# Kernel tuning notes

Measured on AMD Instinct MI355X. Metric: run time of the kernel, lower is better.

Reference implementation:

```python
import jax, jax.numpy as jnp
import numpy as np


def setup_inputs() -> dict:
    key = jax.random.key(0)
    k_u, k_ev, k_lam = jax.random.split(key, 3)
    B, K, L = 64, 32, 8192
    u = jax.random.normal(k_u, (B, L), dtype=jnp.float32)
    # synthetic stand-in for load_or_compute_eigen_data
    eigenvectors = jax.random.normal(k_ev, (K, L), dtype=jnp.float32)
    # module stores eigenvalues ** 0.25
    eigenvalues = jax.random.uniform(k_lam, (K,), dtype=jnp.float32) ** 0.25
    return {"u": u, "eigenvectors": eigenvectors, "eigenvalues": eigenvalues}


def reference(u, eigenvectors, eigenvalues):
    L = u.shape[-1]
    u_fft = jnp.fft.rfft(u)                    # (B, L//2+1) complex
    ev_fft = jnp.fft.rfft(eigenvectors)        # (K, L//2+1) complex (precomputed param in torch)
    # NOTE: faithful to torch einsum 'bi,kj->bkj' which SUMS over i
    p_fft = jnp.einsum('bi,kj->bkj', u_fft, ev_fft)   # (B, K, L//2+1)
    convolutions = jnp.fft.irfft(p_fft, n=L)           # (B, K, L)
    result = jnp.einsum('bkl,k->bl', convolutions, eigenvalues)  # (B, L)
    return result
```

## Files before the change

kernel.cpp:

```cpp
#include <hip/hip_runtime.h>
#include <math.h>

constexpr int Lc = 8192;
constexpr int Kc = 32;
constexpr int Bc = 64;
constexpr int NSLICE = 32;
constexpr int NCHUNK = 8;

__device__ inline float cot_pi_frac_f(int d) {
    int dd = d; float s = 1.0f;
    if (dd > Lc / 2) { dd = Lc - dd; s = -1.0f; }
    float ang = (float)(M_PI * (double)dd / (double)Lc);
    return s * __fdividef(__cosf(ang), __sinf(ang));
}


__global__ __launch_bounds__(256) void k_w(
    const float* __restrict__ ev, const float* __restrict__ lam,
    float* __restrict__ wbuf)
{
    const int n = blockIdx.x * 256 + threadIdx.x;
    float wv = 0.f;
#pragma unroll
    for (int k = 0; k < Kc; ++k)
        wv = fmaf(lam[k], ev[(size_t)k * Lc + n], wv);
    wbuf[n] = wv;
}

__global__ __launch_bounds__(256) void k_main(
    const float* __restrict__ u, const float* __restrict__ wbuf,
    float* __restrict__ sr, float* __restrict__ si2, float* __restrict__ Bp)
{
    const int t = threadIdx.x;

    if (blockIdx.x < 64) {
        int b = blockIdx.x;
        const float4* u4 = (const float4*)(u + (size_t)b * Lc);
        float ar0 = 0.f, ar1 = 0.f, ai0 = 0.f, ai1 = 0.f;
#pragma unroll
        for (int i = 0; i < 8; ++i) {
            int j = t + 256 * i;
            float4 v = u4[j];
            ar0 += v.x; ar1 += v.z;
            ai0 = fmaf(v.y, cot_pi_frac_f(4 * j + 1), ai0);
            ai1 = fmaf(v.w, cot_pi_frac_f(4 * j + 3), ai1);
        }
        if (t == 0) ar0 += 4096.0f * u[(size_t)b * Lc];
        float ar = ar0 + ar1, ai = ai0 + ai1;
        for (int off = 32; off > 0; off >>= 1) {
            ar += __shfl_down(ar, off);
            ai += __shfl_down(ai, off);
        }
        __shared__ float red[8];
        int wave = t >> 6, lane = t & 63;
        if (lane == 0) { red[wave] = ar; red[4 + wave] = ai; }
        __syncthreads();
        if (t == 0) {
            sr[b]  = red[0] + red[1] + red[2] + red[3];
            si2[b] = (2.0f / (float)Lc) * (red[4] + red[5] + red[6] + red[7]);
        }
        return;
    }

    __shared__ float s_we[643];
    __shared__ float s_wo[643];
    __shared__ __align__(16) float s_c[128];

    const int blk = blockIdx.x - 64;
    const int cn = blk & (NCHUNK - 1);
    const int sl = blk >> 3;
    const int n0 = cn * 1024;
    const int dbase = sl * 256;
    const int A = n0 - dbase - 256;

#pragma unroll
    for (int it = 0; it < 2; ++it) {
        int gq = t + 256 * it;
        if (gq < 320) {
            int pos = (A + 4 * gq + 2 * Lc) & (Lc - 1);
            float4 v = *(const float4*)(wbuf + pos);
            s_we[2 * gq]     = v.x; s_wo[2 * gq]     = v.y;
            s_we[2 * gq + 1] = v.z; s_wo[2 * gq + 1] = v.w;
        }
    }
    if (t < 128) s_c[t] = cot_pi_frac_f(dbase + 255 - 2 * t);
    __syncthreads();

    const int g = t >> 1, p = t & 1;
    const float* s_wp = p ? (s_we + 1) : s_wo;
    const int jb = 4 * g;

    float W0 = s_wp[jb],     W1 = s_wp[jb + 1], W2 = s_wp[jb + 2], W3 = s_wp[jb + 3];
    float W4 = s_wp[jb + 4], W5 = s_wp[jb + 5], W6 = s_wp[jb + 6];
    float a0 = 0.f, a1 = 0.f, a2 = 0.f, a3 = 0.f;

    const float4* s_c4 = (const float4*)s_c;
#pragma unroll
    for (int G = 0; G < 32; ++G) {
        const int mm0 = 4 * G;
        float4 cv = s_c4[G];
        a0 = fmaf(cv.x, W0, a0); a1 = fmaf(cv.x, W1, a1); a2 = fmaf(cv.x, W2, a2); a3 = fmaf(cv.x, W3, a3);
        a0 = fmaf(cv.y, W1, a0); a1 = fmaf(cv.y, W2, a1); a2 = fmaf(cv.y, W3, a2); a3 = fmaf(cv.y, W4, a3);
        a0 = fmaf(cv.z, W2, a0); a1 = fmaf(cv.z, W3, a1); a2 = fmaf(cv.z, W4, a2); a3 = fmaf(cv.z, W5, a3);
        a0 = fmaf(cv.w, W3, a0); a1 = fmaf(cv.w, W4, a1); a2 = fmaf(cv.w, W5, a2); a3 = fmaf(cv.w, W6, a3);
        if (G < 31) {
            W0 = W4; W1 = W5; W2 = W6;
            W3 = s_wp[jb + mm0 + 7];  W4 = s_wp[jb + mm0 + 8];
            W5 = s_wp[jb + mm0 + 9];  W6 = s_wp[jb + mm0 + 10];
        }
    }
    float* dst = Bp + (size_t)sl * Lc + n0 + 8 * g + p;
    dst[0] = a0; dst[2] = a1; dst[4] = a2; dst[6] = a3;
}

__global__ __launch_bounds__(256) void k_out(
    const float* __restrict__ wbuf,
    const float* __restrict__ sr, const float* __restrict__ si2,
    const float* __restrict__ Bp, float* __restrict__ out)
{
    __shared__ float s_sv[128];
    const int t = threadIdx.x;
    if (t < 128) s_sv[t] = (t < 64) ? sr[t] : si2[t - 64];
    const int cn = blockIdx.x & 31, bg = blockIdx.x >> 5;
    const int n = cn * 256 + t;
    float wv = wbuf[n];
    float bsum = 0.f;
#pragma unroll
    for (int s = 0; s < NSLICE; ++s) bsum += Bp[(size_t)s * Lc + n];
    __syncthreads();
#pragma unroll
    for (int j = 0; j < 8; ++j) {
        int b = bg * 8 + j;
        out[(size_t)b * Lc + n] = fmaf(s_sv[b], wv, s_sv[64 + b] * bsum);
    }
}

extern "C" void kernel_launch(void* const* d_in, const int* in_sizes, int n_in,
                              void* d_out, int out_size, void* d_ws, size_t ws_size,
                              hipStream_t stream) {
    const float* u   = (const float*)d_in[0];
    const float* ev  = (const float*)d_in[1];
    const float* lam = (const float*)d_in[2];
    float* out = (float*)d_out;

    float* ws   = (float*)d_ws;
    float* sr   = ws;
    float* si2  = ws + 64;
    float* wbuf = ws + 128;
    float* Bp   = ws + 128 + Lc;

    hipLaunchKernelGGL(k_w,    dim3(Lc / 256), dim3(256), 0, stream, ev, lam, wbuf);
    hipLaunchKernelGGL(k_main, dim3(64 + NCHUNK * NSLICE), dim3(256), 0, stream,
                       u, wbuf, sr, si2, Bp);
    hipLaunchKernelGGL(k_out,  dim3(256), dim3(256), 0, stream,
                       wbuf, sr, si2, Bp, out);
}
```

Before: 64.46 us.

## Fuse three kernels into one cooperative kernel with grid-wide syncs

Merges the weight-reduction, main correlation and output kernels into a single cooperative launch of 256 blocks, separated by two grid.sync barriers. The u-reduction blocks and the wbuf blocks now run concurrently in phase one. This removes two kernel launch boundaries and their drain/fill gaps. In exchange it adds grid-barrier cost, and the cooperative launch path can carry extra overhead.

```diff
diff --git a/kernel.cpp b/kernel.cpp
--- a/kernel.cpp
+++ b/kernel.cpp
@@ -1,5 +1,8 @@
 #include <hip/hip_runtime.h>
+#include <hip/hip_cooperative_groups.h>
 #include <math.h>
+
+namespace cg = cooperative_groups;
 
 constexpr int Lc = 8192;
 constexpr int Kc = 32;
@@ -15,26 +18,24 @@
 }
 
 
-__global__ __launch_bounds__(256) void k_w(
-    const float* __restrict__ ev, const float* __restrict__ lam,
-    float* __restrict__ wbuf)
+__global__ __launch_bounds__(256) void k_fused(
+    const float* __restrict__ u, const float* __restrict__ ev,
+    const float* __restrict__ lam, float* __restrict__ out,
+    float* __restrict__ sr, float* __restrict__ si2,
+    float* __restrict__ wbuf, float* __restrict__ Bp)
 {
-    const int n = blockIdx.x * 256 + threadIdx.x;
-    float wv = 0.f;
-#pragma unroll
-    for (int k = 0; k < Kc; ++k)
-        wv = fmaf(lam[k], ev[(size_t)k * Lc + n], wv);
-    wbuf[n] = wv;
-}
+    cg::grid_group grid = cg::this_grid();
+    const int t = threadIdx.x;
+    const int blk = blockIdx.x;
 
-__global__ __launch_bounds__(256) void k_main(
-    const float* __restrict__ u, const float* __restrict__ wbuf,
-    float* __restrict__ sr, float* __restrict__ si2, float* __restrict__ Bp)
-{
-    const int t = threadIdx.x;
+    __shared__ float s_we[643];
+    __shared__ float s_wo[643];
+    __shared__ __align__(16) float s_c[128];
+    __shared__ float red[8];
+    __shared__ float s_sv[128];
 
-    if (blockIdx.x < 64) {
-        int b = blockIdx.x;
+    if (blk < 64) {
+        const int b = blk;
         const float4* u4 = (const float4*)(u + (size_t)b * Lc);
         float ar0 = 0.f, ar1 = 0.f, ai0 = 0.f, ai1 = 0.f;
 #pragma unroll
@@ -51,7 +52,6 @@
             ar += __shfl_down(ar, off);
             ai += __shfl_down(ai, off);
         }
-        __shared__ float red[8];
         int wave = t >> 6, lane = t & 63;
         if (lane == 0) { red[wave] = ar; red[4 + wave] = ai; }
         __syncthreads();
@@ -59,79 +59,80 @@
             sr[b]  = red[0] + red[1] + red[2] + red[3];
             si2[b] = (2.0f / (float)Lc) * (red[4] + red[5] + red[6] + red[7]);
         }
-        return;
+    } else if (blk < 96) {
+        const int n = (blk - 64) * 256 + t;
+        float wv = 0.f;
+#pragma unroll
+        for (int k = 0; k < Kc; ++k)
+            wv = fmaf(lam[k], ev[(size_t)k * Lc + n], wv);
+        wbuf[n] = wv;
     }
 
-    __shared__ float s_we[643];
-    __shared__ float s_wo[643];
-    __shared__ __align__(16) float s_c[128];
+    grid.sync();
 
-    const int blk = blockIdx.x - 64;
-    const int cn = blk & (NCHUNK - 1);
-    const int sl = blk >> 3;
-    const int n0 = cn * 1024;
-    const int dbase = sl * 256;
-    const int A = n0 - dbase - 256;
+    {
+        const int cn = blk & (NCHUNK - 1);
+        const int sl = blk >> 3;
+        const int n0 = cn * 1024;
+        const int dbase = sl * 256;
+        const int A = n0 - dbase - 256;
 
 #pragma unroll
-    for (int it = 0; it < 2; ++it) {
-        int gq = t + 256 * it;
-        if (gq < 320) {
-            int pos = (A + 4 * gq + 2 * Lc) & (Lc - 1);
-            float4 v = *(const float4*)(wbuf + pos);
-            s_we[2 * gq]     = v.x; s_wo[2 * gq]     = v.y;
-            s_we[2 * gq + 1] = v.z; s_wo[2 * gq + 1] = v.w;
+        for (int it = 0; it < 2; ++it) {
+            int gq = t + 256 * it;
+            if (gq < 320) {
+                int pos = (A + 4 * gq + 2 * Lc) & (Lc - 1);
+                float4 v = *(const float4*)(wbuf + pos);
+                s_we[2 * gq]     = v.x; s_wo[2 * gq]     = v.y;
+                s_we[2 * gq + 1] = v.z; s_wo[2 * gq + 1] = v.w;
+            }
         }
+        if (t < 128) s_c[t] = cot_pi_frac_f(dbase + 255 - 2 * t);
+        __syncthreads();
+
+        const int g = t >> 1, p = t & 1;
+        const float* s_wp = p ? (s_we + 1) : s_wo;
+        const int jb = 4 * g;
+
+        float W0 = s_wp[jb],     W1 = s_wp[jb + 1], W2 = s_wp[jb + 2], W3 = s_wp[jb + 3];
+        float W4 = s_wp[jb + 4], W5 = s_wp[jb + 5], W6 = s_wp[jb + 6];
+        float a0 = 0.f, a1 = 0.f, a2 = 0.f, a3 = 0.f;
+
+        const float4* s_c4 = (const float4*)s_c;
+#pragma unroll
+        for (int G = 0; G < 32; ++G) {
+            const int mm0 = 4 * G;
+            float4 cv = s_c4[G];
+            a0 = fmaf(cv.x, W0, a0); a1 = fmaf(cv.x, W1, a1); a2 = fmaf(cv.x, W2, a2); a3 = fmaf(cv.x, W3, a3);
+            a0 = fmaf(cv.y, W1, a0); a1 = fmaf(cv.y, W2, a1); a2 = fmaf(cv.y, W3, a2); a3 = fmaf(cv.y, W4, a3);
+            a0 = fmaf(cv.z, W2, a0); a1 = fmaf(cv.z, W3, a1); a2 = fmaf(cv.z, W4, a2); a3 = fmaf(cv.z, W5, a3);
+            a0 = fmaf(cv.w, W3, a0); a1 = fmaf(cv.w, W4, a1); a2 = fmaf(cv.w, W5, a2); a3 = fmaf(cv.w, W6, a3);
+            if (G < 31) {
+                W0 = W4; W1 = W5; W2 = W6;
+                W3 = s_wp[jb + mm0 + 7];  W4 = s_wp[jb + mm0 + 8];
+                W5 = s_wp[jb + mm0 + 9];  W6 = s_wp[jb + mm0 + 10];
+            }
+        }
+        float* dst = Bp + (size_t)sl * Lc + n0 + 8 * g + p;
+        dst[0] = a0; dst[2] = a1; dst[4] = a2; dst[6] = a3;
     }
-    if (t < 128) s_c[t] = cot_pi_frac_f(dbase + 255 - 2 * t);
-    __syncthreads();
 
-    const int g = t >> 1, p = t & 1;
-    const float* s_wp = p ? (s_we + 1) : s_wo;
-    const int jb = 4 * g;
+    grid.sync();
 
-    float W0 = s_wp[jb],     W1 = s_wp[jb + 1], W2 = s_wp[jb + 2], W3 = s_wp[jb + 3];
-    float W4 = s_wp[jb + 4], W5 = s_wp[jb + 5], W6 = s_wp[jb + 6];
-    float a0 = 0.f, a1 = 0.f, a2 = 0.f, a3 = 0.f;
-
-    const float4* s_c4 = (const float4*)s_c;
+    {
+        if (t < 128) s_sv[t] = (t < 64) ? sr[t] : si2[t - 64];
+        const int cn = blk & 31, bg = blk >> 5;
+        const int n = cn * 256 + t;
+        float wv = wbuf[n];
+        float bsum = 0.f;
 #pragma unroll
-    for (int G = 0; G < 32; ++G) {
-        const int mm0 = 4 * G;
-        float4 cv = s_c4[G];
-        a0 = fmaf(cv.x, W0, a0); a1 = fmaf(cv.x, W1, a1); a2 = fmaf(cv.x, W2, a2); a3 = fmaf(cv.x, W3, a3);
-        a0 = fmaf(cv.y, W1, a0); a1 = fmaf(cv.y, W2, a1); a2 = fmaf(cv.y, W3, a2); a3 = fmaf(cv.y, W4, a3);
-        a0 = fmaf(cv.z, W2, a0); a1 = fmaf(cv.z, W3, a1); a2 = fmaf(cv.z, W4, a2); a3 = fmaf(cv.z, W5, a3);
-        a0 = fmaf(cv.w, W3, a0); a1 = fmaf(cv.w, W4, a1); a2 = fmaf(cv.w, W5, a2); a3 = fmaf(cv.w, W6, a3);
-        if (G < 31) {
-            W0 = W4; W1 = W5; W2 = W6;
-            W3 = s_wp[jb + mm0 + 7];  W4 = s_wp[jb + mm0 + 8];
-            W5 = s_wp[jb + mm0 + 9];  W6 = s_wp[jb + mm0 + 10];
+        for (int s = 0; s < NSLICE; ++s) bsum += Bp[(size_t)s * Lc + n];
+        __syncthreads();
+#pragma unroll
+        for (int j = 0; j < 8; ++j) {
+            int b = bg * 8 + j;
+            out[(size_t)b * Lc + n] = fmaf(s_sv[b], wv, s_sv[64 + b] * bsum);
         }
-    }
-    float* dst = Bp + (size_t)sl * Lc + n0 + 8 * g + p;
-    dst[0] = a0; dst[2] = a1; dst[4] = a2; dst[6] = a3;
-}
-
-__global__ __launch_bounds__(256) void k_out(
-    const float* __restrict__ wbuf,
-    const float* __restrict__ sr, const float* __restrict__ si2,
-    const float* __restrict__ Bp, float* __restrict__ out)
-{
-    __shared__ float s_sv[128];
-    const int t = threadIdx.x;
-    if (t < 128) s_sv[t] = (t < 64) ? sr[t] : si2[t - 64];
-    const int cn = blockIdx.x & 31, bg = blockIdx.x >> 5;
-    const int n = cn * 256 + t;
-    float wv = wbuf[n];
-    float bsum = 0.f;
-#pragma unroll
-    for (int s = 0; s < NSLICE; ++s) bsum += Bp[(size_t)s * Lc + n];
-    __syncthreads();
-#pragma unroll
-    for (int j = 0; j < 8; ++j) {
-        int b = bg * 8 + j;
-        out[(size_t)b * Lc + n] = fmaf(s_sv[b], wv, s_sv[64 + b] * bsum);
     }
 }
 
@@ -149,9 +150,8 @@
     float* wbuf = ws + 128;
     float* Bp   = ws + 128 + Lc;
 
-    hipLaunchKernelGGL(k_w,    dim3(Lc / 256), dim3(256), 0, stream, ev, lam, wbuf);
-    hipLaunchKernelGGL(k_main, dim3(64 + NCHUNK * NSLICE), dim3(256), 0, stream,
-                       u, wbuf, sr, si2, Bp);
-    hipLaunchKernelGGL(k_out,  dim3(256), dim3(256), 0, stream,
-                       wbuf, sr, si2, Bp, out);
+    void* args[] = { (void*)&u, (void*)&ev, (void*)&lam, (void*)&out,
+                     (void*)&sr, (void*)&si2, (void*)&wbuf, (void*)&Bp };
+    hipLaunchCooperativeKernel((void*)k_fused, dim3(256), dim3(256),
+                               args, 0, stream);
 }
```

Result: slower. 132.8 us (+106.1%).

## Regroup kernels: fuse u-reductions with w computation, vectorize conv LDS reads

Applied to the files above, without the earlier changes.

The per-batch u reductions move out of the conv kernel into a new pre-kernel that also computes the lambda-weighted eigenvector sum, so the conv kernel runs only convolution blocks. Shared-memory buffers are laid out so each thread reads its weights as aligned float4 loads from LDS instead of four scalar loads per step. The number of launches stays the same, but the reduction blocks now run alongside the w computation rather than competing with conv blocks, and the inner loop issues fewer LDS instructions.

```diff
diff --git a/kernel.cpp b/kernel.cpp
--- a/kernel.cpp
+++ b/kernel.cpp
@@ -15,24 +15,12 @@
 }
 
 
-__global__ __launch_bounds__(256) void k_w(
-    const float* __restrict__ ev, const float* __restrict__ lam,
-    float* __restrict__ wbuf)
-{
-    const int n = blockIdx.x * 256 + threadIdx.x;
-    float wv = 0.f;
-#pragma unroll
-    for (int k = 0; k < Kc; ++k)
-        wv = fmaf(lam[k], ev[(size_t)k * Lc + n], wv);
-    wbuf[n] = wv;
-}
-
-__global__ __launch_bounds__(256) void k_main(
-    const float* __restrict__ u, const float* __restrict__ wbuf,
-    float* __restrict__ sr, float* __restrict__ si2, float* __restrict__ Bp)
+__global__ __launch_bounds__(256) void k_pre(
+    const float* __restrict__ u, const float* __restrict__ ev,
+    const float* __restrict__ lam, float* __restrict__ sr,
+    float* __restrict__ si2, float* __restrict__ wbuf)
 {
     const int t = threadIdx.x;
-
     if (blockIdx.x < 64) {
         int b = blockIdx.x;
         const float4* u4 = (const float4*)(u + (size_t)b * Lc);
@@ -59,16 +47,26 @@
             sr[b]  = red[0] + red[1] + red[2] + red[3];
             si2[b] = (2.0f / (float)Lc) * (red[4] + red[5] + red[6] + red[7]);
         }
-        return;
+    } else {
+        const int n = (blockIdx.x - 64) * 256 + t;
+        float wv = 0.f;
+#pragma unroll
+        for (int k = 0; k < Kc; ++k)
+            wv = fmaf(lam[k], ev[(size_t)k * Lc + n], wv);
+        wbuf[n] = wv;
     }
+}
 
-    __shared__ float s_we[643];
-    __shared__ float s_wo[643];
+__global__ __launch_bounds__(256) void k_conv(
+    const float* __restrict__ wbuf, float* __restrict__ Bp)
+{
+    __shared__ __align__(16) float s_w0[644];
+    __shared__ __align__(16) float s_w1[644];
     __shared__ __align__(16) float s_c[128];
 
-    const int blk = blockIdx.x - 64;
-    const int cn = blk & (NCHUNK - 1);
-    const int sl = blk >> 3;
+    const int t = threadIdx.x;
+    const int cn = blockIdx.x & (NCHUNK - 1);
+    const int sl = blockIdx.x >> 3;
     const int n0 = cn * 1024;
     const int dbase = sl * 256;
     const int A = n0 - dbase - 256;
@@ -79,35 +77,31 @@
         if (gq < 320) {
             int pos = (A + 4 * gq + 2 * Lc) & (Lc - 1);
             float4 v = *(const float4*)(wbuf + pos);
-            s_we[2 * gq]     = v.x; s_wo[2 * gq]     = v.y;
-            s_we[2 * gq + 1] = v.z; s_wo[2 * gq + 1] = v.w;
+            s_w0[2 * gq]     = v.y;
+            s_w0[2 * gq + 1] = v.w;
+            s_w1[2 * gq]     = v.z;
+            if (gq > 0) s_w1[2 * gq - 1] = v.x;
         }
     }
     if (t < 128) s_c[t] = cot_pi_frac_f(dbase + 255 - 2 * t);
     __syncthreads();
 
     const int g = t >> 1, p = t & 1;
-    const float* s_wp = p ? (s_we + 1) : s_wo;
-    const int jb = 4 * g;
+    const float4* s_w4 = (const float4*)(p ? s_w1 : s_w0);
+    const float4* s_c4 = (const float4*)s_c;
 
-    float W0 = s_wp[jb],     W1 = s_wp[jb + 1], W2 = s_wp[jb + 2], W3 = s_wp[jb + 3];
-    float W4 = s_wp[jb + 4], W5 = s_wp[jb + 5], W6 = s_wp[jb + 6];
+    float4 Wa = s_w4[g];
+    float4 Wb = s_w4[g + 1];
     float a0 = 0.f, a1 = 0.f, a2 = 0.f, a3 = 0.f;
 
-    const float4* s_c4 = (const float4*)s_c;
 #pragma unroll
     for (int G = 0; G < 32; ++G) {
-        const int mm0 = 4 * G;
         float4 cv = s_c4[G];
-        a0 = fmaf(cv.x, W0, a0); a1 = fmaf(cv.x, W1, a1); a2 = fmaf(cv.x, W2, a2); a3 = fmaf(cv.x, W3, a3);
-        a0 = fmaf(cv.y, W1, a0); a1 = fmaf(cv.y, W2, a1); a2 = fmaf(cv.y, W3, a2); a3 = fmaf(cv.y, W4, a3);
-        a0 = fmaf(cv.z, W2, a0); a1 = fmaf(cv.z, W3, a1); a2 = fmaf(cv.z, W4, a2); a3 = fmaf(cv.z, W5, a3);
-        a0 = fmaf(cv.w, W3, a0); a1 = fmaf(cv.w, W4, a1); a2 = fmaf(cv.w, W5, a2); a3 = fmaf(cv.w, W6, a3);
-        if (G < 31) {
-            W0 = W4; W1 = W5; W2 = W6;
-            W3 = s_wp[jb + mm0 + 7];  W4 = s_wp[jb + mm0 + 8];
-            W5 = s_wp[jb + mm0 + 9];  W6 = s_wp[jb + mm0 + 10];
-        }
+        a0 = fmaf(cv.x, Wa.x, a0); a0 = fmaf(cv.y, Wa.y, a0); a0 = fmaf(cv.z, Wa.z, a0); a0 = fmaf(cv.w, Wa.w, a0);
+        a1 = fmaf(cv.x, Wa.y, a1); a1 = fmaf(cv.y, Wa.z, a1); a1 = fmaf(cv.z, Wa.w, a1); a1 = fmaf(cv.w, Wb.x, a1);
+        a2 = fmaf(cv.x, Wa.z, a2); a2 = fmaf(cv.y, Wa.w, a2); a2 = fmaf(cv.z, Wb.x, a2); a2 = fmaf(cv.w, Wb.y, a2);
+        a3 = fmaf(cv.x, Wa.w, a3); a3 = fmaf(cv.y, Wb.x, a3); a3 = fmaf(cv.z, Wb.y, a3); a3 = fmaf(cv.w, Wb.z, a3);
+        if (G < 31) { Wa = Wb; Wb = s_w4[g + G + 2]; }
     }
     float* dst = Bp + (size_t)sl * Lc + n0 + 8 * g + p;
     dst[0] = a0; dst[2] = a1; dst[4] = a2; dst[6] = a3;
@@ -149,9 +143,10 @@
     float* wbuf = ws + 128;
     float* Bp   = ws + 128 + Lc;
 
-    hipLaunchKernelGGL(k_w,    dim3(Lc / 256), dim3(256), 0, stream, ev, lam, wbuf);
-    hipLaunchKernelGGL(k_main, dim3(64 + NCHUNK * NSLICE), dim3(256), 0, stream,
-                       u, wbuf, sr, si2, Bp);
+    hipLaunchKernelGGL(k_pre,  dim3(96),  dim3(256), 0, stream,
+                       u, ev, lam, sr, si2, wbuf);
+    hipLaunchKernelGGL(k_conv, dim3(NCHUNK * NSLICE), dim3(256), 0, stream,
+                       wbuf, Bp);
     hipLaunchKernelGGL(k_out,  dim3(256), dim3(256), 0, stream,
                        wbuf, sr, si2, Bp, out);
 }
```

After: 65.33 us. About the same (+1.4%).
